# Kernel optimization log

Hardware: AMD Instinct MI355X
Metric: run time of the kernel (lower is better)

## Reference

```python
import jax, jax.numpy as jnp
import numpy as np

NUM_HEADS = 4
D_MODEL = 192
NEG_INF = -1000000000.0  # fp32 branch of the original mask fill


def setup_inputs() -> dict:
    key = jax.random.key(0)
    ks = jax.random.split(key, 9)
    b, s, d = 4, 2048, D_MODEL
    inp = {
        "query": jax.random.normal(ks[0], (b, s, d), dtype=jnp.float32),
        "key": jax.random.normal(ks[1], (b, s, d), dtype=jnp.float32),
        "value": jax.random.normal(ks[2], (b, s, d), dtype=jnp.float32),
        "attn_mask": jax.random.randint(ks[3], (b, s, s), 0, 2, dtype=jnp.int32),
        "bias": jax.random.normal(ks[4], (1, NUM_HEADS, s, s), dtype=jnp.float32) * 0.1,
        # nn.Linear(d, d, bias=False) weights, applied as x @ W.T
        "Wq": jax.random.normal(ks[5], (d, d), dtype=jnp.float32) / np.sqrt(d),
        "Wk": jax.random.normal(ks[6], (d, d), dtype=jnp.float32) / np.sqrt(d),
        "Wv": jax.random.normal(ks[7], (d, d), dtype=jnp.float32) / np.sqrt(d),
        "Wo": jax.random.normal(ks[8], (d, d), dtype=jnp.float32) / np.sqrt(d),
    }
    return inp


def reference(query, key, value, attn_mask, bias, Wq, Wk, Wv, Wo):
    b, s, d = query.shape
    h, dh = NUM_HEADS, d // NUM_HEADS
    # QKV projections (Linear, no bias): x @ W.T
    q = (query @ Wq.T).reshape(b, s, h, dh)   # [b,s,h,dh]
    k = (key @ Wk.T).reshape(b, s, h, dh)
    v = (value @ Wv.T).reshape(b, s, h, dh)
    # unscaled dot-product logits (original has no 1/sqrt(d) scaling)
    logits = jnp.einsum("bqhd,bkhd->bhqk", q, k)
    logits = logits + bias                       # bias added BEFORE mask fill
    mask4 = attn_mask[:, None, :, :]             # [b,1,q,k] -> broadcast over heads
    logits = jnp.where(mask4 == 0, NEG_INF, logits)
    weights = jax.nn.softmax(logits, axis=-1)    # [b,h,q,k]
    # dropout_rate=0.0 (eval-mode / identity dropout)
    out = jnp.einsum("bhqk,bkhd->bqhd", weights, v).reshape(b, s, d)
    out = out @ Wo.T
    return out, weights.mean(axis=1)             # ([b,s,d], [b,s,s])
```

## Files before the change

kernel.cpp:

```cpp
#include <hip/hip_runtime.h>

#define BB 4
#define SS 2048
#define HH 4
#define DD 192
#define QT 16
#define NT (SS / 2 / 64)
#define NEG_BIG (-1e9f)
#define MB_NEG 0xCE6Eu

typedef __attribute__((ext_vector_type(8))) short short8;
typedef __attribute__((ext_vector_type(4))) float f32x4;

__device__ inline ushort f2bf(float x) {
    union { float f; unsigned u; } v; v.f = x;
    unsigned r = (v.u + 0x7FFFu + ((v.u >> 16) & 1u)) >> 16;
    return (ushort)r;
}
__device__ inline float bf2f(ushort x) {
    union { unsigned u; float f; } v; v.u = ((unsigned)x) << 16;
    return v.f;
}
__device__ inline void wave_lds_fence() {
    __builtin_amdgcn_wave_barrier();
    __builtin_amdgcn_s_waitcnt(0xC07F);
    __builtin_amdgcn_wave_barrier();
}

__global__ __launch_bounds__(256) void wt_kernel(
    const float* __restrict__ Wq, const float* __restrict__ Wk,
    const float* __restrict__ Wv, const float* __restrict__ Wo,
    float* __restrict__ WTall)
{
    __shared__ float tile[32][33];
    const float* W = (blockIdx.z == 0) ? Wq : (blockIdx.z == 1) ? Wk
                   : (blockIdx.z == 2) ? Wv : Wo;
    float* WT = WTall + (size_t)blockIdx.z * DD * DD;
    const int c0 = blockIdx.x * 32, j0 = blockIdx.y * 32;
    const int tx = threadIdx.x & 31, ty = threadIdx.x >> 5;
#pragma unroll
    for (int k = 0; k < 4; ++k)
        tile[ty + 8 * k][tx] = W[(size_t)(j0 + ty + 8 * k) * DD + c0 + tx];
    __syncthreads();
#pragma unroll
    for (int k = 0; k < 4; ++k)
        WT[(size_t)(c0 + ty + 8 * k) * DD + j0 + tx] = tile[tx][ty + 8 * k];
}

__global__ __launch_bounds__(192) void qkv_proj_kernel(
    const float* __restrict__ Xq, const float* __restrict__ Xk,
    const float* __restrict__ Xv, const float* __restrict__ WTall,
    ushort* __restrict__ qpad, ushort* __restrict__ kpad,
    ushort* __restrict__ vT)
{
    const int mode = blockIdx.y;
    const float* __restrict__ X = (mode == 0) ? Xq : (mode == 1) ? Xk : Xv;
    const float* __restrict__ WT = WTall + (size_t)mode * DD * DD;

    __shared__ __align__(16) float xs[32][DD];
    const int row0 = blockIdx.x * 32;
    const int t = threadIdx.x;
    {
        const float4* src = (const float4*)(X + (size_t)row0 * DD);
        float4* dst = (float4*)&xs[0][0];
        for (int i = t; i < 32 * DD / 4; i += 192) dst[i] = src[i];
    }
    __syncthreads();

    const int jt = (t % 48) * 4;
    const int rowg = t / 48;

    float acc[8][4];
#pragma unroll
    for (int r = 0; r < 8; ++r)
#pragma unroll
        for (int j = 0; j < 4; ++j) acc[r][j] = 0.f;

#pragma unroll 2
    for (int k4 = 0; k4 < DD / 4; ++k4) {
        float4 w0 = *(const float4*)&WT[(size_t)(k4 * 4 + 0) * DD + jt];
        float4 w1 = *(const float4*)&WT[(size_t)(k4 * 4 + 1) * DD + jt];
        float4 w2 = *(const float4*)&WT[(size_t)(k4 * 4 + 2) * DD + jt];
        float4 w3 = *(const float4*)&WT[(size_t)(k4 * 4 + 3) * DD + jt];
#pragma unroll
        for (int r = 0; r < 8; ++r) {
            float4 xv = *(const float4*)&xs[rowg * 8 + r][k4 * 4];
            acc[r][0] = fmaf(xv.x, w0.x, acc[r][0]); acc[r][1] = fmaf(xv.x, w0.y, acc[r][1]);
            acc[r][2] = fmaf(xv.x, w0.z, acc[r][2]); acc[r][3] = fmaf(xv.x, w0.w, acc[r][3]);
            acc[r][0] = fmaf(xv.y, w1.x, acc[r][0]); acc[r][1] = fmaf(xv.y, w1.y, acc[r][1]);
            acc[r][2] = fmaf(xv.y, w1.z, acc[r][2]); acc[r][3] = fmaf(xv.y, w1.w, acc[r][3]);
            acc[r][0] = fmaf(xv.z, w2.x, acc[r][0]); acc[r][1] = fmaf(xv.z, w2.y, acc[r][1]);
            acc[r][2] = fmaf(xv.z, w2.z, acc[r][2]); acc[r][3] = fmaf(xv.z, w2.w, acc[r][3]);
            acc[r][0] = fmaf(xv.w, w3.x, acc[r][0]); acc[r][1] = fmaf(xv.w, w3.y, acc[r][1]);
            acc[r][2] = fmaf(xv.w, w3.z, acc[r][2]); acc[r][3] = fmaf(xv.w, w3.w, acc[r][3]);
        }
    }

    if (mode < 2) {
        ushort* __restrict__ out = (mode == 0) ? qpad : kpad;
        const int hd = jt / 48, f = jt % 48;
#pragma unroll
        for (int r = 0; r < 8; ++r) {
            ushort4 o;
            o.x = f2bf(acc[r][0]); o.y = f2bf(acc[r][1]);
            o.z = f2bf(acc[r][2]); o.w = f2bf(acc[r][3]);
            *(ushort4*)&out[((size_t)(row0 + rowg * 8 + r) * HH + hd) * 64 + f] = o;
        }
        const int4 z = make_int4(0, 0, 0, 0);
        for (int i = t; i < 256; i += 192) {
            const int row = i >> 3, hh = (i >> 1) & 3, half = i & 1;
            *(int4*)&out[((size_t)(row0 + row) * HH + hh) * 64 + 48 + half * 8] = z;
        }
    } else {
        const int b = row0 >> 11, s0 = row0 & (SS - 1);
#pragma unroll
        for (int j = 0; j < 4; ++j) {
            const int col = jt + j, hd = col / 48, f = col % 48;
#pragma unroll
            for (int p = 0; p < 4; ++p) {
                unsigned pk = (unsigned)f2bf(acc[2 * p][j]) |
                              ((unsigned)f2bf(acc[2 * p + 1][j]) << 16);
                *(unsigned*)&vT[(((size_t)b * HH + hd) * 48 + f) * SS +
                                s0 + rowg * 8 + 2 * p] = pk;
            }
        }
    }
}

__global__ __launch_bounds__(192) void o_proj_kernel(
    const float* __restrict__ X, const float* __restrict__ WT,
    float* __restrict__ Y)
{
    __shared__ __align__(16) float xs[32][DD];
    const int row0 = blockIdx.x * 32;
    const int t = threadIdx.x;
    {
        const float4* src = (const float4*)(X + (size_t)row0 * DD);
        float4* dst = (float4*)&xs[0][0];
        for (int i = t; i < 32 * DD / 4; i += 192) dst[i] = src[i];
    }
    __syncthreads();

    const int jt = (t % 48) * 4;
    const int rowg = t / 48;

    float acc[8][4];
#pragma unroll
    for (int r = 0; r < 8; ++r)
#pragma unroll
        for (int j = 0; j < 4; ++j) acc[r][j] = 0.f;

#pragma unroll 2
    for (int k4 = 0; k4 < DD / 4; ++k4) {
        float4 w0 = *(const float4*)&WT[(size_t)(k4 * 4 + 0) * DD + jt];
        float4 w1 = *(const float4*)&WT[(size_t)(k4 * 4 + 1) * DD + jt];
        float4 w2 = *(const float4*)&WT[(size_t)(k4 * 4 + 2) * DD + jt];
        float4 w3 = *(const float4*)&WT[(size_t)(k4 * 4 + 3) * DD + jt];
#pragma unroll
        for (int r = 0; r < 8; ++r) {
            float4 xv = *(const float4*)&xs[rowg * 8 + r][k4 * 4];
            acc[r][0] = fmaf(xv.x, w0.x, acc[r][0]); acc[r][1] = fmaf(xv.x, w0.y, acc[r][1]);
            acc[r][2] = fmaf(xv.x, w0.z, acc[r][2]); acc[r][3] = fmaf(xv.x, w0.w, acc[r][3]);
            acc[r][0] = fmaf(xv.y, w1.x, acc[r][0]); acc[r][1] = fmaf(xv.y, w1.y, acc[r][1]);
            acc[r][2] = fmaf(xv.y, w1.z, acc[r][2]); acc[r][3] = fmaf(xv.y, w1.w, acc[r][3]);
            acc[r][0] = fmaf(xv.z, w2.x, acc[r][0]); acc[r][1] = fmaf(xv.z, w2.y, acc[r][1]);
            acc[r][2] = fmaf(xv.z, w2.z, acc[r][2]); acc[r][3] = fmaf(xv.z, w2.w, acc[r][3]);
            acc[r][0] = fmaf(xv.w, w3.x, acc[r][0]); acc[r][1] = fmaf(xv.w, w3.y, acc[r][1]);
            acc[r][2] = fmaf(xv.w, w3.z, acc[r][2]); acc[r][3] = fmaf(xv.w, w3.w, acc[r][3]);
        }
    }

#pragma unroll
    for (int r = 0; r < 8; ++r)
        *(float4*)&Y[(size_t)(row0 + rowg * 8 + r) * DD + jt] =
            make_float4(acc[r][0], acc[r][1], acc[r][2], acc[r][3]);
}

__device__ inline f32x4 qk_tile(const ushort* kp, short8 qa0, short8 qa1) {
    short8 kb0 = *(const short8*)(kp);
    short8 kb1 = *(const short8*)(kp + 32);
    f32x4 d = {0.f, 0.f, 0.f, 0.f};
    d = __builtin_amdgcn_mfma_f32_16x16x32_bf16(qa0, kb0, d, 0, 0, 0);
    d = __builtin_amdgcn_mfma_f32_16x16x32_bf16(qa1, kb1, d, 0, 0, 0);
    return d;
}

__global__ __launch_bounds__(512, 4) void attn_kernel(
    const ushort* __restrict__ qpad, const ushort* __restrict__ kpad,
    const ushort* __restrict__ vT, const int* __restrict__ mask,
    const float* __restrict__ bias,
    ushort* __restrict__ wscr, float* __restrict__ linv_g,
    float* __restrict__ oattn)
{
    __shared__ __align__(16) ushort wb[8][QT][72];
    __shared__ float l_scr[8][QT];

    const int b  = blockIdx.x >> 7;
    const int q0 = (blockIdx.x & 127) * QT;
    const int t = threadIdx.x;
    const int w = t >> 6;
    const int h = w & 3;
    const int kh = w >> 2;
    const int lane = t & 63;
    const int n16 = lane & 15, quad = lane >> 4;
    const int kbase0 = kh * (SS / 2);

    const ushort* qbase =
        qpad + ((size_t)(b * SS + q0 + n16) * HH + h) * 64 + quad * 8;
    const short8 qa0 = *(const short8*)(qbase);
    const short8 qa1 = *(const short8*)(qbase + 32);
    const ushort* kbase = kpad + (size_t)b * SS * HH * 64 + h * 64 + quad * 8;

    const int srow = lane >> 4;
    const int skey = (lane & 15) * 4;
    const int* mrow0 = mask + (size_t)(b * SS + q0) * SS + kbase0 + skey;
    const float* brow0 = bias + (size_t)(h * SS + q0) * SS + kbase0 + skey;

    float l_[4] = {0.f, 0.f, 0.f, 0.f};
    f32x4 pv[3];
#pragma unroll
    for (int nb = 0; nb < 3; ++nb) pv[nb] = (f32x4){0.f, 0.f, 0.f, 0.f};

    int4  mzc[4];
    float4 bvc[4];
#pragma unroll
    for (int rr = 0; rr < 4; ++rr) {
        const int row = rr * 4 + srow;
        mzc[rr] = *(const int4*)(mrow0 + (size_t)row * SS);
        bvc[rr] = *(const float4*)(brow0 + (size_t)row * SS);
    }

    for (int kt = 0; kt < NT; ++kt) {
        const int kb = kt * 64;
#pragma unroll
        for (int rr = 0; rr < 4; ++rr) {
            const int row = rr * 4 + srow;
            ushort4 o;
            o.x = mzc[rr].x ? f2bf(bvc[rr].x) : (ushort)MB_NEG;
            o.y = mzc[rr].y ? f2bf(bvc[rr].y) : (ushort)MB_NEG;
            o.z = mzc[rr].z ? f2bf(bvc[rr].z) : (ushort)MB_NEG;
            o.w = mzc[rr].w ? f2bf(bvc[rr].w) : (ushort)MB_NEG;
            *(ushort4*)&wb[w][row][skey] = o;
        }
        if (kt + 1 < NT) {
#pragma unroll
            for (int rr = 0; rr < 4; ++rr) {
                const int row = rr * 4 + srow;
                mzc[rr] = *(const int4*)(mrow0 + (size_t)row * SS + kb + 64);
                bvc[rr] = *(const float4*)(brow0 + (size_t)row * SS + kb + 64);
            }
        }
        wave_lds_fence();

#pragma unroll
        for (int g = 0; g < 4; ++g) {
            const int key = kbase0 + kb + g * 16 + n16;
            f32x4 d = qk_tile(kbase + (size_t)key * (HH * 64), qa0, qa1);
#pragma unroll
            for (int r = 0; r < 4; ++r) {
                float wgt = __expf(d[r] + bf2f(wb[w][quad * 4 + r][g * 16 + n16]));
                l_[r] += wgt;
                wb[w][quad * 4 + r][g * 16 + n16] = f2bf(wgt);
            }
        }
        wave_lds_fence();

        const short8 wa0 = *(const short8*)&wb[w][n16][quad * 8];
        const short8 wa1 = *(const short8*)&wb[w][n16][32 + quad * 8];
#pragma unroll
        for (int nb = 0; nb < 3; ++nb) {
            const ushort* vb = vT + ((size_t)(b * HH + h) * 48 + nb * 16 + n16) * SS
                               + kbase0 + kb + quad * 8;
            short8 v0 = *(const short8*)(vb);
            short8 v1 = *(const short8*)(vb + 32);
            pv[nb] = __builtin_amdgcn_mfma_f32_16x16x32_bf16(wa0, v0, pv[nb], 0, 0, 0);
            pv[nb] = __builtin_amdgcn_mfma_f32_16x16x32_bf16(wa1, v1, pv[nb], 0, 0, 0);
        }

        {
            const int r4 = lane >> 4;
            const int k4 = (lane & 15) * 4;
#pragma unroll
            for (int it = 0; it < 4; ++it) {
                const int row = it * 4 + r4;
                ushort4 wv = *(const ushort4*)&wb[w][row][k4];
                *(ushort4*)&wscr[((size_t)(b * SS + q0 + row) * HH + h) * SS +
                                 kbase0 + kb + k4] = wv;
            }
        }
        wave_lds_fence();
    }

#pragma unroll
    for (int r = 0; r < 4; ++r) {
        float ll = l_[r];
#pragma unroll
        for (int off = 1; off < 16; off <<= 1) ll += __shfl_xor(ll, off);
        l_[r] = ll;
    }
    if (n16 == 0) {
#pragma unroll
        for (int r = 0; r < 4; ++r) l_scr[w][quad * 4 + r] = l_[r];
    }

    __syncthreads();

    float* scr = (float*)&wb[0][0][0];
    if (kh == 1) {
#pragma unroll
        for (int nb = 0; nb < 3; ++nb)
            *(f32x4*)&scr[((size_t)(h * 64 + lane)) * 12 + nb * 4] = pv[nb];
    }
    __syncthreads();

    if (kh == 0) {
        float linv[4];
#pragma unroll
        for (int r = 0; r < 4; ++r)
            linv[r] = 1.0f / (l_scr[h][quad * 4 + r] + l_scr[h + 4][quad * 4 + r]);
        if (n16 == 0) {
#pragma unroll
            for (int r = 0; r < 4; ++r)
                linv_g[((size_t)b * HH + h) * SS + q0 + quad * 4 + r] = linv[r];
        }
#pragma unroll
        for (int nb = 0; nb < 3; ++nb) {
            f32x4 po = *(const f32x4*)&scr[((size_t)(h * 64 + lane)) * 12 + nb * 4];
#pragma unroll
            for (int r = 0; r < 4; ++r)
                oattn[((size_t)(b * SS + q0 + quad * 4 + r)) * DD +
                      h * 48 + nb * 16 + n16] = (pv[nb][r] + po[r]) * linv[r];
        }
    }
}

__global__ __launch_bounds__(256) void out1_kernel(
    const ushort* __restrict__ wscr, const float* __restrict__ linv_g,
    float* __restrict__ out1)
{
    const int bq = blockIdx.x;
    const int b = bq >> 11;
    const int q = bq & (SS - 1);
    const int t = threadIdx.x;
    const ushort* base = wscr + (size_t)bq * (HH * SS) + t * 8;

    float li[HH];
#pragma unroll
    for (int hh = 0; hh < HH; ++hh)
        li[hh] = linv_g[((size_t)b * HH + hh) * SS + q] * 0.25f;

    float acc[8];
#pragma unroll
    for (int j = 0; j < 8; ++j) acc[j] = 0.f;

#pragma unroll
    for (int hh = 0; hh < HH; ++hh) {
        short8 wv = *(const short8*)(base + (size_t)hh * SS);
#pragma unroll
        for (int j = 0; j < 8; ++j)
            acc[j] = fmaf(bf2f((ushort)wv[j]), li[hh], acc[j]);
    }

    float* dst = out1 + (size_t)bq * SS + t * 8;
    *(float4*)dst = make_float4(acc[0], acc[1], acc[2], acc[3]);
    *(float4*)(dst + 4) = make_float4(acc[4], acc[5], acc[6], acc[7]);
}

extern "C" void kernel_launch(void* const* d_in, const int* in_sizes, int n_in,
                              void* d_out, int out_size, void* d_ws, size_t ws_size,
                              hipStream_t stream)
{
    const float* query = (const float*)d_in[0];
    const float* key   = (const float*)d_in[1];
    const float* value = (const float*)d_in[2];
    const int*   amask = (const int*)d_in[3];
    const float* bias  = (const float*)d_in[4];
    const float* Wq    = (const float*)d_in[5];
    const float* Wk    = (const float*)d_in[6];
    const float* Wv    = (const float*)d_in[7];
    const float* Wo    = (const float*)d_in[8];

    const size_t n_rows = (size_t)BB * SS;
    float* out0 = (float*)d_out;
    float* out1 = out0 + n_rows * DD;

    ushort* qpad  = (ushort*)d_ws;
    ushort* kpad  = qpad + n_rows * HH * 64;
    ushort* vT    = kpad + n_rows * HH * 64;
    float*  oattn = (float*)(vT + (size_t)BB * HH * 48 * SS);
    float*  WTall = oattn + n_rows * DD;
    float*  linvg = WTall + 4 * DD * DD;
    ushort* wscr  = (ushort*)(linvg + (size_t)BB * HH * SS);

    wt_kernel<<<dim3(6, 6, 4), 256, 0, stream>>>(Wq, Wk, Wv, Wo, WTall);

    qkv_proj_kernel<<<dim3(n_rows / 32, 3), 192, 0, stream>>>(
        query, key, value, WTall, qpad, kpad, vT);

    attn_kernel<<<dim3(BB * SS / QT), 512, 0, stream>>>(
        qpad, kpad, vT, amask, bias, wscr, linvg, oattn);

    out1_kernel<<<dim3(BB * SS), 256, 0, stream>>>(wscr, linvg, out1);

    o_proj_kernel<<<dim3(n_rows / 32), 192, 0, stream>>>(
        oattn, WTall + 3 * DD * DD, out0);
}
```

Measured before the change: 423.0 us.

## Split attention key range across two blocks with atomic accumulation and separate normalization

```diff
diff --git a/kernel.cpp b/kernel.cpp
--- a/kernel.cpp
+++ b/kernel.cpp
@@ -5,7 +5,7 @@
 #define HH 4
 #define DD 192
 #define QT 16
-#define NT (SS / 2 / 64)
+#define NT (SS / 4 / 64)
 #define NEG_BIG (-1e9f)
 #define MB_NEG 0xCE6Eu
 
@@ -25,6 +25,11 @@
     __builtin_amdgcn_wave_barrier();
     __builtin_amdgcn_s_waitcnt(0xC07F);
     __builtin_amdgcn_wave_barrier();
+}
+
+__global__ __launch_bounds__(256) void zero_kernel(float4* __restrict__ p)
+{
+    p[(size_t)blockIdx.x * 256 + threadIdx.x] = make_float4(0.f, 0.f, 0.f, 0.f);
 }
 
 __global__ __launch_bounds__(256) void wt_kernel(
@@ -185,11 +190,11 @@
     return d;
 }
 
-__global__ __launch_bounds__(512, 4) void attn_kernel(
+__global__ __launch_bounds__(512, 8) void attn_kernel(
     const ushort* __restrict__ qpad, const ushort* __restrict__ kpad,
     const ushort* __restrict__ vT, const int* __restrict__ mask,
     const float* __restrict__ bias,
-    ushort* __restrict__ wscr, float* __restrict__ linv_g,
+    ushort* __restrict__ wscr, float* __restrict__ lsum,
     float* __restrict__ oattn)
 {
     __shared__ __align__(16) ushort wb[8][QT][72];
@@ -197,13 +202,14 @@
 
     const int b  = blockIdx.x >> 7;
     const int q0 = (blockIdx.x & 127) * QT;
+    const int hb = blockIdx.y;
     const int t = threadIdx.x;
     const int w = t >> 6;
     const int h = w & 3;
-    const int kh = w >> 2;
+    const int kk = w >> 2;
     const int lane = t & 63;
     const int n16 = lane & 15, quad = lane >> 4;
-    const int kbase0 = kh * (SS / 2);
+    const int kbase0 = (hb * 2 + kk) * (SS / 4);
 
     const ushort* qbase =
         qpad + ((size_t)(b * SS + q0 + n16) * HH + h) * 64 + quad * 8;
@@ -306,32 +312,47 @@
     __syncthreads();
 
     float* scr = (float*)&wb[0][0][0];
-    if (kh == 1) {
+    if (kk == 1) {
 #pragma unroll
         for (int nb = 0; nb < 3; ++nb)
             *(f32x4*)&scr[((size_t)(h * 64 + lane)) * 12 + nb * 4] = pv[nb];
+    } else if (n16 == 0) {
+#pragma unroll
+        for (int r = 0; r < 4; ++r) {
+            float lhalf = l_scr[h][quad * 4 + r] + l_scr[h + 4][quad * 4 + r];
+            atomicAdd(&lsum[((size_t)b * HH + h) * SS + q0 + quad * 4 + r], lhalf);
+        }
     }
     __syncthreads();
 
-    if (kh == 0) {
-        float linv[4];
-#pragma unroll
-        for (int r = 0; r < 4; ++r)
-            linv[r] = 1.0f / (l_scr[h][quad * 4 + r] + l_scr[h + 4][quad * 4 + r]);
-        if (n16 == 0) {
-#pragma unroll
-            for (int r = 0; r < 4; ++r)
-                linv_g[((size_t)b * HH + h) * SS + q0 + quad * 4 + r] = linv[r];
-        }
+    if (kk == 0) {
 #pragma unroll
         for (int nb = 0; nb < 3; ++nb) {
             f32x4 po = *(const f32x4*)&scr[((size_t)(h * 64 + lane)) * 12 + nb * 4];
 #pragma unroll
             for (int r = 0; r < 4; ++r)
-                oattn[((size_t)(b * SS + q0 + quad * 4 + r)) * DD +
-                      h * 48 + nb * 16 + n16] = (pv[nb][r] + po[r]) * linv[r];
-        }
-    }
+                atomicAdd(&oattn[((size_t)(b * SS + q0 + quad * 4 + r)) * DD +
+                                 h * 48 + nb * 16 + n16], pv[nb][r] + po[r]);
+        }
+    }
+}
+
+__global__ __launch_bounds__(256) void norm_kernel(
+    float* __restrict__ oattn, const float* __restrict__ lsum,
+    float* __restrict__ linv_g)
+{
+    const int i4 = blockIdx.x * 256 + threadIdx.x;
+    const int row = i4 / (DD / 4);
+    const int c4 = i4 - row * (DD / 4);
+    const int d0 = c4 * 4;
+    const int h = d0 / 48;
+    const int b = row >> 11, q = row & (SS - 1);
+    const float linv = 1.0f / lsum[((size_t)b * HH + h) * SS + q];
+    float4 v = *(float4*)&oattn[(size_t)row * DD + d0];
+    v.x *= linv; v.y *= linv; v.z *= linv; v.w *= linv;
+    *(float4*)&oattn[(size_t)row * DD + d0] = v;
+    if ((d0 % 48) == 0)
+        linv_g[((size_t)b * HH + h) * SS + q] = linv;
 }
 
 __global__ __launch_bounds__(256) void out1_kernel(
@@ -388,17 +409,24 @@
     ushort* kpad  = qpad + n_rows * HH * 64;
     ushort* vT    = kpad + n_rows * HH * 64;
     float*  oattn = (float*)(vT + (size_t)BB * HH * 48 * SS);
-    float*  WTall = oattn + n_rows * DD;
+    float*  lsum  = oattn + n_rows * DD;
+    float*  WTall = lsum + (size_t)BB * HH * SS;
     float*  linvg = WTall + 4 * DD * DD;
     ushort* wscr  = (ushort*)(linvg + (size_t)BB * HH * SS);
 
+    zero_kernel<<<dim3((n_rows * DD + (size_t)BB * HH * SS) / 4 / 256), 256, 0,
+                  stream>>>((float4*)oattn);
+
     wt_kernel<<<dim3(6, 6, 4), 256, 0, stream>>>(Wq, Wk, Wv, Wo, WTall);
 
     qkv_proj_kernel<<<dim3(n_rows / 32, 3), 192, 0, stream>>>(
         query, key, value, WTall, qpad, kpad, vT);
 
-    attn_kernel<<<dim3(BB * SS / QT), 512, 0, stream>>>(
-        qpad, kpad, vT, amask, bias, wscr, linvg, oattn);
+    attn_kernel<<<dim3(BB * SS / QT, 2), 512, 0, stream>>>(
+        qpad, kpad, vT, amask, bias, wscr, lsum, oattn);
+
+    norm_kernel<<<dim3(n_rows * DD / 4 / 256), 256, 0, stream>>>(
+        oattn, lsum, linvg);
 
     out1_kernel<<<dim3(BB * SS), 256, 0, stream>>>(wscr, linvg, out1);
 
```

After: 664.8 us. 1.57x slower.
